# Performance work log

Hardware: AMD Instinct MI355X
Metric: run time of the kernel (lower is better)

The kernel has to match this reference:

```python
import jax, jax.numpy as jnp
import numpy as np

B, H, O, E, CMAP = 8192, 1024, 256, 16, 1000


def setup_inputs() -> dict:
    key = jax.random.key(0)
    k_x, k_w, k_b, k_num, k_c = jax.random.split(key, 5)
    x = jax.random.normal(k_x, (B, H), dtype=jnp.float32)
    num = jax.random.randint(k_num, (B,), 0, CMAP, dtype=jnp.int64)
    c = jax.random.randint(k_c, (CMAP,), 0, E, dtype=jnp.int64)
    # per-expert Linear params (torch default: uniform(-1/sqrt(H), 1/sqrt(H)))
    bound = 1.0 / np.sqrt(H)
    W = jax.random.uniform(k_w, (E, O, H), dtype=jnp.float32, minval=-bound, maxval=bound)
    b = jax.random.uniform(k_b, (E, O), dtype=jnp.float32, minval=-bound, maxval=bound)
    return {"x": x, "W": W, "b": b, "num": num, "c": c}


def reference(x, W, b, num, c):
    # expert id for each sample: layers[c[num[i]]]
    expert = c[num]  # [B]
    # compute all experts' linear outputs in one batched GEMM, then select.
    # logits: [B, E, O]
    logits = jnp.einsum('bh,eoh->beo', x, W) + b[None, :, :]
    sel = jnp.take_along_axis(logits, expert[:, None, None], axis=1)[:, 0, :]  # [B, O]
    return jax.nn.sigmoid(sel)
```

## Files before the change

kernel.cpp:

```cpp
#include <hip/hip_runtime.h>
#include <stdint.h>

#define B_N   8192
#define H_K   1024
#define O_N   256
#define E_N   16
#define RCAP  1024

#define TILE_M    32
#define TILE_N    128
#define BK        64
#define NITER     (H_K / BK)
#define MTILES    (RCAP / TILE_M)

#define WS_CURSOR   0
#define WS_ROWBUF   1024
#define WS_WBF16    131072

typedef __attribute__((ext_vector_type(8))) short  short8;
typedef __attribute__((ext_vector_type(4))) float  float4v;

__device__ __forceinline__ short f32_to_bf16(float f) {
    uint32_t u = __builtin_bit_cast(uint32_t, f);
    u += 0x7fffu + ((u >> 16) & 1u);
    return (short)(u >> 16);
}

__device__ __forceinline__ short8 cvt8(float4v v0, float4v v1) {
    short8 s;
    s[0] = f32_to_bf16(v0[0]); s[1] = f32_to_bf16(v0[1]);
    s[2] = f32_to_bf16(v0[2]); s[3] = f32_to_bf16(v0[3]);
    s[4] = f32_to_bf16(v1[0]); s[5] = f32_to_bf16(v1[1]);
    s[6] = f32_to_bf16(v1[2]); s[7] = f32_to_bf16(v1[3]);
    return s;
}

__device__ __forceinline__ float4v mfma16(short8 a, short8 b, float4v c) {
    return __builtin_amdgcn_mfma_f32_16x16x32_bf16(a, b, c, 0, 0, 0);
}

__device__ __forceinline__ void gl2lds16(const void* gsrc, void* ldst) {
    __builtin_amdgcn_global_load_lds(
        (const __attribute__((address_space(1))) uint32_t*)gsrc,
        (__attribute__((address_space(3))) uint32_t*)ldst, 16, 0, 0);
}

__global__ __launch_bounds__(256) void
k_prep(const float* __restrict__ W, const int* __restrict__ num, const int* __restrict__ c,
       int* __restrict__ cursor, int* __restrict__ rowbuf, short* __restrict__ Wb) {
    const int tid = threadIdx.x;
    const int bx  = blockIdx.x;

    if (bx < E_N) {
        unsigned mask = 0;
#pragma unroll
        for (int u = 0; u < 32; ++u) {
            const int i = u * 256 + tid;
            const int e = c[num[i]];
            mask |= (unsigned)(e == bx) << u;
        }
        const int cnt = __popc(mask);
        const int lane = tid & 63, wv = tid >> 6;
        int incl = cnt;
#pragma unroll
        for (int d = 1; d < 64; d <<= 1) {
            int v = __shfl_up(incl, d, 64);
            if (lane >= d) incl += v;
        }
        __shared__ int wsum[4];
        if (lane == 63) wsum[wv] = incl;
        __syncthreads();
        int base = 0;
        for (int w = 0; w < wv; ++w) base += wsum[w];
        int pos = base + incl - cnt;
        for (int u = 0; u < 32; ++u)
            if ((mask >> u) & 1u) rowbuf[bx * RCAP + pos++] = u * 256 + tid;
        if (tid == 255) cursor[bx] = base + incl;
    } else {
        const int nchunk = E_N * O_N * H_K / 8;
        const int stride = 240 * 256;
        for (int ch = (bx - E_N) * 256 + tid; ch < nchunk; ch += stride) {
            const float4v* src = (const float4v*)(W + (size_t)ch * 8);
            *(short8*)(Wb + (size_t)ch * 8) = cvt8(src[0], src[1]);
        }
    }
}

__global__ __launch_bounds__(256, 4) void
k_gemm(const float* __restrict__ x, const short* __restrict__ Wb,
       const float* __restrict__ bias, const int* __restrict__ cursor,
       const int* __restrict__ rowbuf, float* __restrict__ out) {
    const int e = blockIdx.x;
    int count = cursor[e]; if (count > RCAP) count = RCAP;
    const int m0 = blockIdx.y * TILE_M;
    if (m0 >= count) return;
    const int n0 = blockIdx.z * TILE_N;

    __shared__ short xs[2][TILE_M][BK];
    __shared__ short wsh[2][TILE_N][BK];

    const int tid = threadIdx.x;
    const int r8  = tid >> 3;
    const int c8  = tid & 7;
    const int xrow = (m0 + r8 < count) ? rowbuf[e * RCAP + m0 + r8] : -1;
    const int xphys = (c8 ^ (r8 & 7)) * 8;

    const int lane = tid & 63;
    const int wave = tid >> 6;
    const int quad = lane >> 4, l16 = lane & 15;

    const int sub = lane >> 3;
    const int clx = (lane & 7) ^ sub;

    const short* wseg = Wb + (size_t)(e * O_N + n0) * H_K;

    float4v xv0, xv1;
    auto load_x = [&](int k0) {
        if (xrow >= 0) {
            const float4v* p = (const float4v*)(x + (size_t)xrow * H_K + k0 + c8 * 8);
            xv0 = p[0]; xv1 = p[1];
        } else { xv0 = (float4v)0.0f; xv1 = (float4v)0.0f; }
    };
    auto store_x = [&](int buf) {
        *(short8*)&xs[buf][r8][xphys] = cvt8(xv0, xv1);
    };
    auto issue_w = [&](int buf, int k0) {
#pragma unroll
        for (int u = 0; u < 4; ++u) {
            const int q = wave * 4 + u;
            gl2lds16(wseg + (size_t)(q * 8 + sub) * H_K + k0 + clx * 8,
                     &wsh[buf][q * 8][0]);
        }
    };

    float4v acc[2][2];
#pragma unroll
    for (int i = 0; i < 2; ++i)
#pragma unroll
        for (int j = 0; j < 2; ++j) acc[i][j] = (float4v)0.0f;

    load_x(0);
    issue_w(0, 0);
    store_x(0);

    for (int k = 0; k < NITER; ++k) {
        const int cur = k & 1;
        __syncthreads();
        if (k + 1 < NITER) {
            load_x((k + 1) * BK);
            issue_w(1 - cur, (k + 1) * BK);
        }

#pragma unroll
        for (int ks = 0; ks < 2; ++ks) {
            const int cl = ks * 4 + quad;
            const int cx = (cl ^ (l16 & 7)) * 8;
            short8 a0 = *(const short8*)&xs[cur][l16][cx];
            short8 a1 = *(const short8*)&xs[cur][16 + l16][cx];
            short8 b0 = *(const short8*)&wsh[cur][wave * 32 + l16][cx];
            short8 b1 = *(const short8*)&wsh[cur][wave * 32 + 16 + l16][cx];
            acc[0][0] = mfma16(a0, b0, acc[0][0]);
            acc[0][1] = mfma16(a0, b1, acc[0][1]);
            acc[1][0] = mfma16(a1, b0, acc[1][0]);
            acc[1][1] = mfma16(a1, b1, acc[1][1]);
        }

        if (k + 1 < NITER) store_x(1 - cur);
    }

#pragma unroll
    for (int ch = 0; ch < 2; ++ch) {
        const int colg = n0 + wave * 32 + ch * 16 + l16;
        const float bv = bias[e * O_N + colg];
#pragma unroll
        for (int rh = 0; rh < 2; ++rh) {
#pragma unroll
            for (int reg = 0; reg < 4; ++reg) {
                const int pos = m0 + rh * 16 + quad * 4 + reg;
                if (pos < count) {
                    const int rid = rowbuf[e * RCAP + pos];
                    const float v = acc[rh][ch][reg] + bv;
                    out[(size_t)rid * O_N + colg] = 1.0f / (1.0f + __expf(-v));
                }
            }
        }
    }
}

extern "C" void kernel_launch(void* const* d_in, const int* in_sizes, int n_in,
                              void* d_out, int out_size, void* d_ws, size_t ws_size,
                              hipStream_t stream) {
    const float* x   = (const float*)d_in[0];
    const float* W   = (const float*)d_in[1];
    const float* b   = (const float*)d_in[2];
    const int*   num = (const int*)d_in[3];
    const int*   c   = (const int*)d_in[4];
    float* out = (float*)d_out;

    char*  ws     = (char*)d_ws;
    int*   cursor = (int*)(ws + WS_CURSOR);
    int*   rowbuf = (int*)(ws + WS_ROWBUF);
    short* Wb     = (short*)(ws + WS_WBF16);

    k_prep<<<256, 256, 0, stream>>>(W, num, c, cursor, rowbuf, Wb);

    dim3 gg(E_N, MTILES, O_N / TILE_N);
    k_gemm<<<gg, 256, 0, stream>>>(x, Wb, b, cursor, rowbuf, out);
}
```

Measured before the change: 115.3 us.

## Load expert weight fragments directly into registers instead of staging via LDS

Replaces the global-to-LDS async staging of the bf16 weight tile with direct per-lane global loads into a double-buffered register array laid out in MFMA B-operand order. The K loop is fully unrolled so the register buffer indices resolve at compile time. This removes the LDS traffic and LDS footprint for weights, which may raise occupancy, but the global loads are strided across rows (16 bytes per row per lane) and raise register pressure.

```diff
diff --git a/kernel.cpp b/kernel.cpp
--- a/kernel.cpp
+++ b/kernel.cpp
@@ -37,12 +37,6 @@
 
 __device__ __forceinline__ float4v mfma16(short8 a, short8 b, float4v c) {
     return __builtin_amdgcn_mfma_f32_16x16x32_bf16(a, b, c, 0, 0, 0);
-}
-
-__device__ __forceinline__ void gl2lds16(const void* gsrc, void* ldst) {
-    __builtin_amdgcn_global_load_lds(
-        (const __attribute__((address_space(1))) uint32_t*)gsrc,
-        (__attribute__((address_space(3))) uint32_t*)ldst, 16, 0, 0);
 }
 
 __global__ __launch_bounds__(256) void
@@ -97,7 +91,6 @@
     const int n0 = blockIdx.z * TILE_N;
 
     __shared__ short xs[2][TILE_M][BK];
-    __shared__ short wsh[2][TILE_N][BK];
 
     const int tid = threadIdx.x;
     const int r8  = tid >> 3;
@@ -109,10 +102,7 @@
     const int wave = tid >> 6;
     const int quad = lane >> 4, l16 = lane & 15;
 
-    const int sub = lane >> 3;
-    const int clx = (lane & 7) ^ sub;
-
-    const short* wseg = Wb + (size_t)(e * O_N + n0) * H_K;
+    const short* bbase = Wb + (size_t)(e * O_N + n0 + wave * 32 + l16) * H_K + quad * 8;
 
     float4v xv0, xv1;
     auto load_x = [&](int k0) {
@@ -124,13 +114,15 @@
     auto store_x = [&](int buf) {
         *(short8*)&xs[buf][r8][xphys] = cvt8(xv0, xv1);
     };
-    auto issue_w = [&](int buf, int k0) {
-#pragma unroll
-        for (int u = 0; u < 4; ++u) {
-            const int q = wave * 4 + u;
-            gl2lds16(wseg + (size_t)(q * 8 + sub) * H_K + k0 + clx * 8,
-                     &wsh[buf][q * 8][0]);
-        }
+
+    short8 breg[2][2][2];
+    auto load_b = [&](int buf, int k0) {
+#pragma unroll
+        for (int f = 0; f < 2; ++f)
+#pragma unroll
+            for (int ks = 0; ks < 2; ++ks)
+                breg[buf][f][ks] =
+                    *(const short8*)(bbase + (size_t)f * 16 * H_K + ks * 32 + k0);
     };
 
     float4v acc[2][2];
@@ -140,15 +132,16 @@
         for (int j = 0; j < 2; ++j) acc[i][j] = (float4v)0.0f;
 
     load_x(0);
-    issue_w(0, 0);
+    load_b(0, 0);
     store_x(0);
 
+#pragma unroll
     for (int k = 0; k < NITER; ++k) {
         const int cur = k & 1;
         __syncthreads();
         if (k + 1 < NITER) {
             load_x((k + 1) * BK);
-            issue_w(1 - cur, (k + 1) * BK);
+            load_b(1 - cur, (k + 1) * BK);
         }
 
 #pragma unroll
@@ -157,20 +150,18 @@
             const int cx = (cl ^ (l16 & 7)) * 8;
             short8 a0 = *(const short8*)&xs[cur][l16][cx];
             short8 a1 = *(const short8*)&xs[cur][16 + l16][cx];
-            short8 b0 = *(const short8*)&wsh[cur][wave * 32 + l16][cx];
-            short8 b1 = *(const short8*)&wsh[cur][wave * 32 + 16 + l16][cx];
-            acc[0][0] = mfma16(a0, b0, acc[0][0]);
-            acc[0][1] = mfma16(a0, b1, acc[0][1]);
-            acc[1][0] = mfma16(a1, b0, acc[1][0]);
-            acc[1][1] = mfma16(a1, b1, acc[1][1]);
+            acc[0][0] = mfma16(a0, breg[cur][0][ks], acc[0][0]);
+            acc[0][1] = mfma16(a0, breg[cur][1][ks], acc[0][1]);
+            acc[1][0] = mfma16(a1, breg[cur][0][ks], acc[1][0]);
+            acc[1][1] = mfma16(a1, breg[cur][1][ks], acc[1][1]);
         }
 
         if (k + 1 < NITER) store_x(1 - cur);
     }
 
 #pragma unroll
-    for (int ch = 0; ch < 2; ++ch) {
-        const int colg = n0 + wave * 32 + ch * 16 + l16;
+    for (int f = 0; f < 2; ++f) {
+        const int colg = n0 + wave * 32 + f * 16 + l16;
         const float bv = bias[e * O_N + colg];
 #pragma unroll
         for (int rh = 0; rh < 2; ++rh) {
@@ -179,7 +170,7 @@
                 const int pos = m0 + rh * 16 + quad * 4 + reg;
                 if (pos < count) {
                     const int rid = rowbuf[e * RCAP + pos];
-                    const float v = acc[rh][ch][reg] + bv;
+                    const float v = acc[rh][f][reg] + bv;
                     out[(size_t)rid * O_N + colg] = 1.0f / (1.0f + __expf(-v));
                 }
             }
```

New measurement: 125.0 us. +8.4%, slower.
